# Optimization experiments

Hardware: AMD Instinct MI355X
Metric: run time of the kernel (lower is better)

Reference implementation:

```python
import jax, jax.numpy as jnp
import numpy as np

EMBED_DIM = 512
NUM_HEADS = 8
HEAD_DIM = EMBED_DIM // NUM_HEADS
N_NODES = 65536
EPS = 1e-5


def setup_inputs() -> dict:
    key = jax.random.key(0)
    ks = jax.random.split(key, 16)
    std = 0.02
    E, F = EMBED_DIM, 4 * EMBED_DIM
    return {
        "x": jax.random.normal(ks[0], (N_NODES, E), jnp.float32),
        "Wq": jax.random.normal(ks[1], (E, E), jnp.float32) * std,
        "bq": jnp.zeros((E,), jnp.float32),
        "Wk": jax.random.normal(ks[2], (E, E), jnp.float32) * std,
        "bk": jnp.zeros((E,), jnp.float32),
        "Wv": jax.random.normal(ks[3], (E, E), jnp.float32) * std,
        "bv": jnp.zeros((E,), jnp.float32),
        "Wo": jax.random.normal(ks[4], (E, E), jnp.float32) * std,
        "bo": jnp.zeros((E,), jnp.float32),
        "W1": jax.random.normal(ks[5], (F, E), jnp.float32) * std,
        "b1": jnp.zeros((F,), jnp.float32),
        "W2": jax.random.normal(ks[6], (E, F), jnp.float32) * std,
        "b2": jnp.zeros((E,), jnp.float32),
        "g1": jnp.ones((E,), jnp.float32),
        "beta1": jnp.zeros((E,), jnp.float32),
        "g2": jnp.ones((E,), jnp.float32),
        "beta2": jnp.zeros((E,), jnp.float32),
    }


def _layernorm(x, g, b):
    mu = jnp.mean(x, axis=-1, keepdims=True)
    var = jnp.mean(jnp.square(x - mu), axis=-1, keepdims=True)
    return (x - mu) * jax.lax.rsqrt(var + EPS) * g + b


def reference(x, Wq, bq, Wk, bk, Wv, bv, Wo, bo, W1, b1, W2, b2, g1, beta1, g2, beta2):
    N = x.shape[0]
    H, D = NUM_HEADS, HEAD_DIM
    residual = x
    h = _layernorm(x, g1, beta1)
    q = (h @ Wq.T + bq).reshape(N, H, D)
    k = (h @ Wk.T + bk).reshape(N, H, D)
    v = (h @ Wv.T + bv).reshape(N, H, D)
    # per-node attention across heads: scores (N, H, H)
    scores = jnp.einsum('nhd,ngd->nhg', q, k) / np.float32(np.sqrt(D))
    attn = jax.nn.softmax(scores, axis=-1)
    out = jnp.einsum('nhg,ngd->nhd', attn, v).reshape(N, H * D)
    out = out @ Wo.T + bo
    x = residual + out  # dropout is identity in eval
    residual = x
    h = _layernorm(x, g2, beta2)
    ff = jax.nn.relu(h @ W1.T + b1) @ W2.T + b2
    return residual + ff
```

## Files before the change

kernel.cpp:

```cpp
#include <hip/hip_runtime.h>
#include <hip/hip_bf16.h>
#include <stdint.h>

typedef __hip_bfloat16 bf16;
typedef short bf16x8 __attribute__((ext_vector_type(8)));
typedef float f32x4 __attribute__((ext_vector_type(4)));

typedef __attribute__((address_space(1))) const unsigned int as1_uint;
typedef __attribute__((address_space(3))) unsigned int as3_uint;

__device__ __forceinline__ void async_copy16(const void* g, void* l) {
    __builtin_amdgcn_global_load_lds((as1_uint*)g, (as3_uint*)l, 16, 0, 0);
}

__device__ __forceinline__ float b2f(unsigned short u) {
    union { unsigned int i; float f; } c; c.i = ((unsigned int)u) << 16; return c.f;
}
__device__ __forceinline__ unsigned short f2b(float f) {
    union { float f; unsigned int i; } c; c.f = f;
    unsigned int i = c.i;
    i += 0x7fffu + ((i >> 16) & 1u);
    return (unsigned short)(i >> 16);
}

__global__ __launch_bounds__(256)
void cvt_kernel(const float* __restrict__ in, bf16* __restrict__ out)
{
    const int i = (blockIdx.x * 256 + threadIdx.x) * 8;
    const float4 a = *(const float4*)(in + i);
    const float4 b = *(const float4*)(in + i + 4);
    union { uint4 v; unsigned short s[8]; } u;
    u.s[0] = f2b(a.x); u.s[1] = f2b(a.y); u.s[2] = f2b(a.z); u.s[3] = f2b(a.w);
    u.s[4] = f2b(b.x); u.s[5] = f2b(b.y); u.s[6] = f2b(b.z); u.s[7] = f2b(b.w);
    *(uint4*)((unsigned short*)out + i) = u.v;
}

__global__ __launch_bounds__(256)
void ln_kernel(const float* __restrict__ x, const float* __restrict__ g,
               const float* __restrict__ beta, bf16* __restrict__ out)
{
    const int w = threadIdx.x >> 6, l = threadIdx.x & 63;
    const int n = blockIdx.x * 4 + w;

    const float* xr = x + (size_t)n * 512 + l * 8;
    const float4 a = *(const float4*)xr;
    const float4 b = *(const float4*)(xr + 4);
    float f[8] = {a.x, a.y, a.z, a.w, b.x, b.y, b.z, b.w};

    float s = 0.f, q = 0.f;
#pragma unroll
    for (int i = 0; i < 8; ++i) { s += f[i]; q += f[i] * f[i]; }
#pragma unroll
    for (int o = 32; o > 0; o >>= 1) { s += __shfl_xor(s, o); q += __shfl_xor(q, o); }
    const float mean = s * (1.f / 512.f);
    const float var  = q * (1.f / 512.f) - mean * mean;
    const float rstd = rsqrtf(var + 1e-5f);

    const float4 g0 = *(const float4*)(g + l * 8);
    const float4 g1 = *(const float4*)(g + l * 8 + 4);
    const float4 b0 = *(const float4*)(beta + l * 8);
    const float4 b1 = *(const float4*)(beta + l * 8 + 4);
    const float gg[8] = {g0.x,g0.y,g0.z,g0.w,g1.x,g1.y,g1.z,g1.w};
    const float bb[8] = {b0.x,b0.y,b0.z,b0.w,b1.x,b1.y,b1.z,b1.w};

    union { uint4 v; unsigned short s[8]; } o;
#pragma unroll
    for (int i = 0; i < 8; ++i)
        o.s[i] = f2b((f[i] - mean) * rstd * gg[i] + bb[i]);
    *(uint4*)((unsigned short*)out + (size_t)n * 512 + l * 8) = o.v;
}

__global__ __launch_bounds__(256)
void attn_kernel(const bf16* __restrict__ qkv, bf16* __restrict__ out)
{
    __shared__ unsigned short sm[4][1536];
    const int w = threadIdx.x >> 6, l = threadIdx.x & 63;
    const int n = blockIdx.x * 4 + w;

    const uint4* src = (const uint4*)((const unsigned short*)qkv + (size_t)n * 1536);
    uint4* dst = (uint4*)sm[w];
#pragma unroll
    for (int i = 0; i < 3; ++i) dst[i * 64 + l] = src[i * 64 + l];
    __syncthreads();

    const int h = l >> 3, gi = l & 7;
    const unsigned short* qrow = sm[w] + h * 64;
    const unsigned short* krow = sm[w] + 512 + gi * 64;
    float s = 0.f;
#pragma unroll
    for (int jj = 0; jj < 8; ++jj) {
        union { uint4 v; unsigned short s8[8]; } qa, ka;
        qa.v = *(const uint4*)(qrow + jj * 8);
        ka.v = *(const uint4*)(krow + jj * 8);
#pragma unroll
        for (int j = 0; j < 8; ++j) s += b2f(qa.s8[j]) * b2f(ka.s8[j]);
    }
    s *= 0.125f;

    float m = s;
#pragma unroll
    for (int o = 1; o < 8; o <<= 1) m = fmaxf(m, __shfl_xor(m, o));
    float e = __expf(s - m);
    float d = e;
#pragma unroll
    for (int o = 1; o < 8; o <<= 1) d += __shfl_xor(d, o);
    const float p = e / d;

    float acc[8];
#pragma unroll
    for (int j = 0; j < 8; ++j) acc[j] = 0.f;
    const int j8 = (l & 7) * 8;
#pragma unroll
    for (int gg = 0; gg < 8; ++gg) {
        const float pg = __shfl(p, (l & 56) | gg);
        union { uint4 v; unsigned short s8[8]; } va;
        va.v = *(const uint4*)(sm[w] + 1024 + gg * 64 + j8);
#pragma unroll
        for (int j = 0; j < 8; ++j) acc[j] += pg * b2f(va.s8[j]);
    }
    union { uint4 v; unsigned short s8[8]; } o;
#pragma unroll
    for (int j = 0; j < 8; ++j) o.s8[j] = f2b(acc[j]);
    *(uint4*)((unsigned short*)out + (size_t)n * 512 + h * 64 + j8) = o.v;
}

#define EPI_PLAIN 0
#define EPI_RES   1
#define EPI_RELU  2

template<int MODE>
__global__ __launch_bounds__(512, 2)
void gemm_bt(const bf16* __restrict__ A,
             const bf16* __restrict__ B0, const bf16* __restrict__ B1,
             const bf16* __restrict__ B2,
             const float* __restrict__ bias0, const float* __restrict__ bias1,
             const float* __restrict__ bias2,
             const float* __restrict__ res,
             void* __restrict__ C,
             int K, int Nper, int ldc)
{
    __shared__ bf16 As[4][8192];
    __shared__ bf16 Bs[4][8192];

    const int tid = threadIdx.x;
    const int w = tid >> 6, l = tid & 63;

    const int nbx = gridDim.x;
    const int nwg = nbx * (int)gridDim.y;
    int lid = blockIdx.y * nbx + blockIdx.x;
    {
        const int q = nwg >> 3, r = nwg & 7;
        const int xcd = lid & 7, idx = lid >> 3;
        lid = (xcd < r ? xcd * (q + 1) : r * (q + 1) + (xcd - r) * q) + idx;
    }
    const int bx = lid % nbx, by = lid / nbx;

    const int rowBase = by * 256;
    const int colBase = bx * 256;
    const int sel = colBase / Nper;
    const bf16*  B    = (sel == 0) ? B0 : (sel == 1) ? B1 : B2;
    const float* bias = (sel == 0) ? bias0 : (sel == 1) ? bias1 : bias2;
    const int colInB = colBase - sel * Nper;

    const bf16* Ag = A + (size_t)rowBase * K;
    const bf16* Bg = B + (size_t)colInB * K;

    const int wr = w >> 2, wc = w & 3;
    const int ml = l & 15;
    const int kc = l >> 4;
    const int ac = ((kc ^ ((ml >> 1) & 3)) << 3);

    auto stage = [&](int t, int slot) {
        const int lr = l >> 2, lc = l & 3;
#pragma unroll
        for (int j = 0; j < 2; ++j) {
            const int cid = w * 2 + j;
            const int r = (cid << 4) + lr;
            const int c = lc ^ ((lr >> 1) & 3);
            const size_t go = (size_t)r * K + (t << 5) + (c << 3);
            async_copy16(Ag + go, &As[slot][cid << 9]);
            async_copy16(Bg + go, &Bs[slot][cid << 9]);
        }
    };

    f32x4 acc[8][4];
#pragma unroll
    for (int i = 0; i < 8; ++i)
#pragma unroll
        for (int j = 0; j < 4; ++j) acc[i][j] = (f32x4)(0.f);

    const int NT = K >> 5;

    stage(0, 0); stage(1, 1); stage(2, 2);
    asm volatile("s_waitcnt vmcnt(8)" ::: "memory");
    __builtin_amdgcn_s_barrier();

    for (int t = 0; t < NT; ++t) {
        if (t + 3 < NT) stage(t + 3, (t + 3) & 3);

        const bf16* Ac = &As[t & 3][0];
        const bf16* Bc = &Bs[t & 3][0];
        bf16x8 bfr[4];
#pragma unroll
        for (int ni = 0; ni < 4; ++ni)
            bfr[ni] = *(const bf16x8*)(Bc + (((wc << 6) + (ni << 4) + ml) << 5) + ac);

        __builtin_amdgcn_s_setprio(1);
#pragma unroll
        for (int mi = 0; mi < 8; ++mi) {
            const bf16x8 a = *(const bf16x8*)(Ac + (((wr << 7) + (mi << 4) + ml) << 5) + ac);
#pragma unroll
            for (int ni = 0; ni < 4; ++ni)
                acc[mi][ni] = __builtin_amdgcn_mfma_f32_16x16x32_bf16(
                    a, bfr[ni], acc[mi][ni], 0, 0, 0);
        }
        __builtin_amdgcn_s_setprio(0);

        if (t < NT - 3)       asm volatile("s_waitcnt vmcnt(8)" ::: "memory");
        else if (t == NT - 3) asm volatile("s_waitcnt vmcnt(4)" ::: "memory");
        else if (t == NT - 2) asm volatile("s_waitcnt vmcnt(0)" ::: "memory");
        if (t < NT - 1) __builtin_amdgcn_s_barrier();
    }

    float bv[4];
#pragma unroll
    for (int ni = 0; ni < 4; ++ni)
        bv[ni] = bias[colInB + (wc << 6) + (ni << 4) + ml];

#pragma unroll
    for (int mi = 0; mi < 8; ++mi) {
#pragma unroll
        for (int r4 = 0; r4 < 4; ++r4) {
            const int row = rowBase + (wr << 7) + (mi << 4) + (kc << 2) + r4;
            const size_t rowoff = (size_t)row * ldc;
#pragma unroll
            for (int ni = 0; ni < 4; ++ni) {
                const int gcol = colBase + (wc << 6) + (ni << 4) + ml;
                float v = acc[mi][ni][r4] + bv[ni];
                if (MODE == EPI_RELU) v = fmaxf(v, 0.f);
                if (MODE == EPI_RES) {
                    v += res[rowoff + gcol];
                    ((float*)C)[rowoff + gcol] = v;
                } else {
                    ((unsigned short*)C)[rowoff + gcol] = f2b(v);
                }
            }
        }
    }
}

extern "C" void kernel_launch(void* const* d_in, const int* in_sizes, int n_in,
                              void* d_out, int out_size, void* d_ws, size_t ws_size,
                              hipStream_t stream)
{
    const float* x   = (const float*)d_in[0];
    const float* Wq  = (const float*)d_in[1];
    const float* bq  = (const float*)d_in[2];
    const float* Wk  = (const float*)d_in[3];
    const float* bk  = (const float*)d_in[4];
    const float* Wv  = (const float*)d_in[5];
    const float* bv  = (const float*)d_in[6];
    const float* Wo  = (const float*)d_in[7];
    const float* bo  = (const float*)d_in[8];
    const float* W1  = (const float*)d_in[9];
    const float* b1  = (const float*)d_in[10];
    const float* W2  = (const float*)d_in[11];
    const float* b2  = (const float*)d_in[12];
    const float* g1  = (const float*)d_in[13];
    const float* be1 = (const float*)d_in[14];
    const float* g2  = (const float*)d_in[15];
    const float* be2 = (const float*)d_in[16];

    const int N = 65536;

    bf16* Wqb = (bf16*)d_ws;
    bf16* Wkb = Wqb + 262144;
    bf16* Wvb = Wkb + 262144;
    bf16* Wob = Wvb + 262144;
    bf16* W1b = Wob + 262144;
    bf16* W2b = W1b + 1048576;
    const size_t wts_bytes = 6ull * 1024 * 1024;
    bf16* t64 = (bf16*)((char*)d_ws + wts_bytes);
    const size_t t64_bytes = (size_t)N * 512 * 2;
    bf16* cb  = (bf16*)((char*)d_ws + wts_bytes + t64_bytes);
    const size_t used = wts_bytes + t64_bytes;
    const size_t avail = ws_size > used ? ws_size - used : 0;
    int Nc = 32768;
    while (Nc > 256 && (size_t)Nc * 4096 > avail) Nc >>= 1;

    float* x2 = (float*)d_out;
    dim3 blk(256);
    dim3 blk5(512);

    cvt_kernel<<<262144 / 2048, blk, 0, stream>>>(Wq, Wqb);
    cvt_kernel<<<262144 / 2048, blk, 0, stream>>>(Wk, Wkb);
    cvt_kernel<<<262144 / 2048, blk, 0, stream>>>(Wv, Wvb);
    cvt_kernel<<<262144 / 2048, blk, 0, stream>>>(Wo, Wob);
    cvt_kernel<<<1048576 / 2048, blk, 0, stream>>>(W1, W1b);
    cvt_kernel<<<1048576 / 2048, blk, 0, stream>>>(W2, W2b);

    ln_kernel<<<N / 4, blk, 0, stream>>>(x, g1, be1, t64);

    for (int r0 = 0; r0 < N; r0 += Nc) {
        gemm_bt<EPI_PLAIN><<<dim3(6, Nc / 256), blk5, 0, stream>>>(
            t64 + (size_t)r0 * 512, Wqb, Wkb, Wvb, bq, bk, bv, nullptr,
            cb, 512, 512, 1536);
        attn_kernel<<<Nc / 4, blk, 0, stream>>>(cb, t64 + (size_t)r0 * 512);
    }

    gemm_bt<EPI_RES><<<dim3(2, N / 256), blk5, 0, stream>>>(
        t64, Wob, Wob, Wob, bo, bo, bo, x, x2, 512, 512, 512);

    ln_kernel<<<N / 4, blk, 0, stream>>>(x2, g2, be2, t64);

    for (int r0 = 0; r0 < N; r0 += Nc) {
        gemm_bt<EPI_RELU><<<dim3(8, Nc / 256), blk5, 0, stream>>>(
            t64 + (size_t)r0 * 512, W1b, W1b, W1b, b1, b1, b1, nullptr,
            cb, 512, 2048, 2048);
        gemm_bt<EPI_RES><<<dim3(2, Nc / 256), blk5, 0, stream>>>(
            cb, W2b, W2b, W2b, b2, b2, b2, x2 + (size_t)r0 * 512,
            x2 + (size_t)r0 * 512, 2048, 512, 512);
    }
}
```

Before: 1.052 ms.

## Split GEMM main loop into two interleaved load/prefetch/MFMA phases

Restructures the bf16 GEMM inner loop into two halves. Each half loads its A fragments from LDS, issues half of the next-tile async global→LDS prefetch, then runs a barrier-synchronised MFMA cluster, in the style of ping-pong scheduling. The aim is to interleave memory issue with matrix compute and let waves alternate between memory and MFMA phases. It adds extra workgroup barriers per K-step, which could cost more than the overlap gains.

```diff
diff --git a/kernel.cpp b/kernel.cpp
--- a/kernel.cpp
+++ b/kernel.cpp
@@ -170,17 +170,14 @@
     const int kc = l >> 4;
     const int ac = ((kc ^ ((ml >> 1) & 3)) << 3);
 
-    auto stage = [&](int t, int slot) {
+    auto stage_half = [&](int t, int slot, int j) {
         const int lr = l >> 2, lc = l & 3;
-#pragma unroll
-        for (int j = 0; j < 2; ++j) {
-            const int cid = w * 2 + j;
-            const int r = (cid << 4) + lr;
-            const int c = lc ^ ((lr >> 1) & 3);
-            const size_t go = (size_t)r * K + (t << 5) + (c << 3);
-            async_copy16(Ag + go, &As[slot][cid << 9]);
-            async_copy16(Bg + go, &Bs[slot][cid << 9]);
-        }
+        const int cid = w * 2 + j;
+        const int r = (cid << 4) + lr;
+        const int c = lc ^ ((lr >> 1) & 3);
+        const size_t go = (size_t)r * K + (t << 5) + (c << 3);
+        async_copy16(Ag + go, &As[slot][cid << 9]);
+        async_copy16(Bg + go, &Bs[slot][cid << 9]);
     };
 
     f32x4 acc[8][4];
@@ -191,29 +188,54 @@
 
     const int NT = K >> 5;
 
-    stage(0, 0); stage(1, 1); stage(2, 2);
+    stage_half(0, 0, 0); stage_half(0, 0, 1);
+    stage_half(1, 1, 0); stage_half(1, 1, 1);
+    stage_half(2, 2, 0); stage_half(2, 2, 1);
     asm volatile("s_waitcnt vmcnt(8)" ::: "memory");
     __builtin_amdgcn_s_barrier();
 
     for (int t = 0; t < NT; ++t) {
-        if (t + 3 < NT) stage(t + 3, (t + 3) & 3);
-
-        const bf16* Ac = &As[t & 3][0];
-        const bf16* Bc = &Bs[t & 3][0];
-        bf16x8 bfr[4];
+        const int slot = t & 3;
+        const bf16* Ac = &As[slot][0];
+        const bf16* Bc = &Bs[slot][0];
+        const bool pf = (t + 3 < NT);
+
+        bf16x8 bfr[4], af[4];
 #pragma unroll
         for (int ni = 0; ni < 4; ++ni)
             bfr[ni] = *(const bf16x8*)(Bc + (((wc << 6) + (ni << 4) + ml) << 5) + ac);
-
+#pragma unroll
+        for (int mi = 0; mi < 4; ++mi)
+            af[mi] = *(const bf16x8*)(Ac + (((wr << 7) + (mi << 4) + ml) << 5) + ac);
+        if (pf) stage_half(t + 3, (t + 3) & 3, 0);
+
+        __builtin_amdgcn_s_barrier();
+        asm volatile("s_waitcnt lgkmcnt(0)" ::: "memory");
         __builtin_amdgcn_s_setprio(1);
 #pragma unroll
-        for (int mi = 0; mi < 8; ++mi) {
-            const bf16x8 a = *(const bf16x8*)(Ac + (((wr << 7) + (mi << 4) + ml) << 5) + ac);
+        for (int mi = 0; mi < 4; ++mi)
 #pragma unroll
             for (int ni = 0; ni < 4; ++ni)
                 acc[mi][ni] = __builtin_amdgcn_mfma_f32_16x16x32_bf16(
-                    a, bfr[ni], acc[mi][ni], 0, 0, 0);
-        }
+                    af[mi], bfr[ni], acc[mi][ni], 0, 0, 0);
+        __builtin_amdgcn_s_setprio(0);
+        __builtin_amdgcn_s_barrier();
+
+        bf16x8 ag[4];
+#pragma unroll
+        for (int mi = 0; mi < 4; ++mi)
+            ag[mi] = *(const bf16x8*)(Ac + (((wr << 7) + ((mi + 4) << 4) + ml) << 5) + ac);
+        if (pf) stage_half(t + 3, (t + 3) & 3, 1);
+
+        __builtin_amdgcn_s_barrier();
+        asm volatile("s_waitcnt lgkmcnt(0)" ::: "memory");
+        __builtin_amdgcn_s_setprio(1);
+#pragma unroll
+        for (int mi = 0; mi < 4; ++mi)
+#pragma unroll
+            for (int ni = 0; ni < 4; ++ni)
+                acc[mi + 4][ni] = __builtin_amdgcn_mfma_f32_16x16x32_bf16(
+                    ag[mi], bfr[ni], acc[mi + 4][ni], 0, 0, 0);
         __builtin_amdgcn_s_setprio(0);
 
         if (t < NT - 3)       asm volatile("s_waitcnt vmcnt(8)" ::: "memory");
```

Result: faster. 985.4 us (-6.3%).

## Shrink GEMM tiles to 128x128 with 256 threads and 3-stage pipeline

Applied to the files above, without the earlier changes.

Reworks the bf16 GEMM from 256x256 tiles on 512 threads with a 4-slot, 3-ahead async LDS pipeline to 128x128 tiles on 256 threads with a 3-slot, 2-ahead pipeline. A fragments are now preloaded per k-step. Launch grids double in each dimension. The aim is a smaller LDS footprint (48KB vs 128KB) and more workgroups per CU to raise occupancy and hide latency. The cost is lower arithmetic intensity per tile, so each output needs more global/L2 traffic, plus a shallower prefetch.

```diff
diff --git a/kernel.cpp b/kernel.cpp
--- a/kernel.cpp
+++ b/kernel.cpp
@@ -129,7 +129,7 @@
 #define EPI_RELU  2
 
 template<int MODE>
-__global__ __launch_bounds__(512, 2)
+__global__ __launch_bounds__(256, 3)
 void gemm_bt(const bf16* __restrict__ A,
              const bf16* __restrict__ B0, const bf16* __restrict__ B1,
              const bf16* __restrict__ B2,
@@ -139,8 +139,8 @@
              void* __restrict__ C,
              int K, int Nper, int ldc)
 {
-    __shared__ bf16 As[4][8192];
-    __shared__ bf16 Bs[4][8192];
+    __shared__ bf16 As[3][4096];
+    __shared__ bf16 Bs[3][4096];
 
     const int tid = threadIdx.x;
     const int w = tid >> 6, l = tid & 63;
@@ -155,8 +155,8 @@
     }
     const int bx = lid % nbx, by = lid / nbx;
 
-    const int rowBase = by * 256;
-    const int colBase = bx * 256;
+    const int rowBase = by * 128;
+    const int colBase = bx * 128;
     const int sel = colBase / Nper;
     const bf16*  B    = (sel == 0) ? B0 : (sel == 1) ? B1 : B2;
     const float* bias = (sel == 0) ? bias0 : (sel == 1) ? bias1 : bias2;
@@ -165,61 +165,63 @@
     const bf16* Ag = A + (size_t)rowBase * K;
     const bf16* Bg = B + (size_t)colInB * K;
 
-    const int wr = w >> 2, wc = w & 3;
+    const int wr = w >> 1, wc = w & 1;
     const int ml = l & 15;
-    const int kc = l >> 4;
-    const int ac = ((kc ^ ((ml >> 1) & 3)) << 3);
+    const int ac = (((l >> 4) ^ ((ml >> 1) & 3)) << 3);
 
     auto stage = [&](int t, int slot) {
         const int lr = l >> 2, lc = l & 3;
-#pragma unroll
-        for (int j = 0; j < 2; ++j) {
-            const int cid = w * 2 + j;
-            const int r = (cid << 4) + lr;
-            const int c = lc ^ ((lr >> 1) & 3);
-            const size_t go = (size_t)r * K + (t << 5) + (c << 3);
-            async_copy16(Ag + go, &As[slot][cid << 9]);
-            async_copy16(Bg + go, &Bs[slot][cid << 9]);
+        const int c = lc ^ ((lr >> 1) & 3);
+#pragma unroll
+        for (int i = 0; i < 2; ++i) {
+            const int base = w * 32 + i * 16;
+            const size_t go = (size_t)(base + lr) * K + (t << 5) + (c << 3);
+            async_copy16(Ag + go, &As[slot][base << 5]);
+            async_copy16(Bg + go, &Bs[slot][base << 5]);
         }
     };
 
-    f32x4 acc[8][4];
-#pragma unroll
-    for (int i = 0; i < 8; ++i)
+    f32x4 acc[4][4];
+#pragma unroll
+    for (int i = 0; i < 4; ++i)
 #pragma unroll
         for (int j = 0; j < 4; ++j) acc[i][j] = (f32x4)(0.f);
 
     const int NT = K >> 5;
 
-    stage(0, 0); stage(1, 1); stage(2, 2);
-    asm volatile("s_waitcnt vmcnt(8)" ::: "memory");
+    stage(0, 0); stage(1, 1);
+    asm volatile("s_waitcnt vmcnt(4)" ::: "memory");
     __builtin_amdgcn_s_barrier();
 
+    int slot = 0, pslot = 2;
     for (int t = 0; t < NT; ++t) {
-        if (t + 3 < NT) stage(t + 3, (t + 3) & 3);
-
-        const bf16* Ac = &As[t & 3][0];
-        const bf16* Bc = &Bs[t & 3][0];
-        bf16x8 bfr[4];
+        if (t + 2 < NT) stage(t + 2, pslot);
+
+        const bf16* Ac = &As[slot][0];
+        const bf16* Bc = &Bs[slot][0];
+        bf16x8 af[4], bfr[4];
+#pragma unroll
+        for (int mi = 0; mi < 4; ++mi)
+            af[mi] = *(const bf16x8*)(Ac + (((wr << 6) + (mi << 4) + ml) << 5) + ac);
 #pragma unroll
         for (int ni = 0; ni < 4; ++ni)
             bfr[ni] = *(const bf16x8*)(Bc + (((wc << 6) + (ni << 4) + ml) << 5) + ac);
 
         __builtin_amdgcn_s_setprio(1);
 #pragma unroll
-        for (int mi = 0; mi < 8; ++mi) {
-            const bf16x8 a = *(const bf16x8*)(Ac + (((wr << 7) + (mi << 4) + ml) << 5) + ac);
+        for (int mi = 0; mi < 4; ++mi)
 #pragma unroll
             for (int ni = 0; ni < 4; ++ni)
                 acc[mi][ni] = __builtin_amdgcn_mfma_f32_16x16x32_bf16(
-                    a, bfr[ni], acc[mi][ni], 0, 0, 0);
-        }
+                    af[mi], bfr[ni], acc[mi][ni], 0, 0, 0);
         __builtin_amdgcn_s_setprio(0);
 
-        if (t < NT - 3)       asm volatile("s_waitcnt vmcnt(8)" ::: "memory");
-        else if (t == NT - 3) asm volatile("s_waitcnt vmcnt(4)" ::: "memory");
+        if (t + 2 < NT)       asm volatile("s_waitcnt vmcnt(4)" ::: "memory");
         else if (t == NT - 2) asm volatile("s_waitcnt vmcnt(0)" ::: "memory");
         if (t < NT - 1) __builtin_amdgcn_s_barrier();
+
+        slot  = (slot  == 2) ? 0 : slot + 1;
+        pslot = (pslot == 2) ? 0 : pslot + 1;
     }
 
     float bv[4];
@@ -228,10 +230,10 @@
         bv[ni] = bias[colInB + (wc << 6) + (ni << 4) + ml];
 
 #pragma unroll
-    for (int mi = 0; mi < 8; ++mi) {
+    for (int mi = 0; mi < 4; ++mi) {
 #pragma unroll
         for (int r4 = 0; r4 < 4; ++r4) {
-            const int row = rowBase + (wr << 7) + (mi << 4) + (kc << 2) + r4;
+            const int row = rowBase + (wr << 6) + (mi << 4) + ((l >> 4) << 2) + r4;
             const size_t rowoff = (size_t)row * ldc;
 #pragma unroll
             for (int ni = 0; ni < 4; ++ni) {
@@ -290,7 +292,6 @@
 
     float* x2 = (float*)d_out;
     dim3 blk(256);
-    dim3 blk5(512);
 
     cvt_kernel<<<262144 / 2048, blk, 0, stream>>>(Wq, Wqb);
     cvt_kernel<<<262144 / 2048, blk, 0, stream>>>(Wk, Wkb);
@@ -302,22 +303,22 @@
     ln_kernel<<<N / 4, blk, 0, stream>>>(x, g1, be1, t64);
 
     for (int r0 = 0; r0 < N; r0 += Nc) {
-        gemm_bt<EPI_PLAIN><<<dim3(6, Nc / 256), blk5, 0, stream>>>(
+        gemm_bt<EPI_PLAIN><<<dim3(12, Nc / 128), blk, 0, stream>>>(
             t64 + (size_t)r0 * 512, Wqb, Wkb, Wvb, bq, bk, bv, nullptr,
             cb, 512, 512, 1536);
         attn_kernel<<<Nc / 4, blk, 0, stream>>>(cb, t64 + (size_t)r0 * 512);
     }
 
-    gemm_bt<EPI_RES><<<dim3(2, N / 256), blk5, 0, stream>>>(
+    gemm_bt<EPI_RES><<<dim3(4, N / 128), blk, 0, stream>>>(
         t64, Wob, Wob, Wob, bo, bo, bo, x, x2, 512, 512, 512);
 
     ln_kernel<<<N / 4, blk, 0, stream>>>(x2, g2, be2, t64);
 
     for (int r0 = 0; r0 < N; r0 += Nc) {
-        gemm_bt<EPI_RELU><<<dim3(8, Nc / 256), blk5, 0, stream>>>(
+        gemm_bt<EPI_RELU><<<dim3(16, Nc / 128), blk, 0, stream>>>(
             t64 + (size_t)r0 * 512, W1b, W1b, W1b, b1, b1, b1, nullptr,
             cb, 512, 2048, 2048);
-        gemm_bt<EPI_RES><<<dim3(2, Nc / 256), blk5, 0, stream>>>(
+        gemm_bt<EPI_RES><<<dim3(4, Nc / 128), blk, 0, stream>>>(
             cb, W2b, W2b, W2b, b2, b2, b2, x2 + (size_t)r0 * 512,
             x2 + (size_t)r0 * 512, 2048, 512, 512);
     }
```

Measured after the change: 1.018 ms. -3.2%, faster.

## Restructure GEMM mainloop into 8-phase ping-pong schedule with 64-wide K tiles

Applied to the files above, without the earlier changes.

The bf16 GEMM mainloop moves from a 4-slot, 32-wide K pipeline to a double-buffered 64-wide K tile split into A/B halves. Each K step is broken into quadrant phases, each with its own LDS fragment loads, async global-to-LDS prefetch, barriers and an MFMA burst, in the style of a ping-pong schedule. The aim is to hide global-load and LDS latency behind matrix work and to halve the loop trip count. It adds more barriers, fragile vmcnt accounting and higher register pressure from the fragment arrays.

```diff
diff --git a/kernel.cpp b/kernel.cpp
--- a/kernel.cpp
+++ b/kernel.cpp
@@ -139,8 +139,8 @@
              void* __restrict__ C,
              int K, int Nper, int ldc)
 {
-    __shared__ bf16 As[4][8192];
-    __shared__ bf16 Bs[4][8192];
+    __shared__ bf16 As[2][2][8192];
+    __shared__ bf16 Bs[2][2][8192];
 
     const int tid = threadIdx.x;
     const int w = tid >> 6, l = tid & 63;
@@ -168,20 +168,34 @@
     const int wr = w >> 2, wc = w & 3;
     const int ml = l & 15;
     const int kc = l >> 4;
-    const int ac = ((kc ^ ((ml >> 1) & 3)) << 3);
-
-    auto stage = [&](int t, int slot) {
-        const int lr = l >> 2, lc = l & 3;
-#pragma unroll
-        for (int j = 0; j < 2; ++j) {
-            const int cid = w * 2 + j;
-            const int r = (cid << 4) + lr;
-            const int c = lc ^ ((lr >> 1) & 3);
-            const size_t go = (size_t)r * K + (t << 5) + (c << 3);
-            async_copy16(Ag + go, &As[slot][cid << 9]);
-            async_copy16(Bg + go, &Bs[slot][cid << 9]);
+    const int rdoff = ((kc ^ ((ml >> 1) & 3)) << 3);
+
+    const int s_row = l >> 2;
+    const int s_koff = (((l & 3) ^ ((l >> 3) & 3)) << 3);
+
+    auto stA = [&](int t, int half) {
+#pragma unroll
+        for (int c = 0; c < 2; ++c) {
+            const int q = (w << 1) | c;
+            const int p = q >> 3, rr = q & 7;
+            const bf16* src = Ag + (size_t)(half * 128 + rr * 16 + s_row) * K
+                            + (t << 6) + p * 32 + s_koff;
+            async_copy16(src, &As[t & 1][half][q << 9]);
         }
     };
+    auto stB = [&](int t, int half) {
+#pragma unroll
+        for (int c = 0; c < 2; ++c) {
+            const int q = (w << 1) | c;
+            const int p = q >> 3, rr = q & 7;
+            const bf16* src = Bg + (size_t)(half * 128 + rr * 16 + s_row) * K
+                            + (t << 6) + p * 32 + s_koff;
+            async_copy16(src, &Bs[t & 1][half][q << 9]);
+        }
+    };
+
+    const int bRow = ((wc & 1) << 6) + ml;
+    const int bHalf = wc >> 1;
 
     f32x4 acc[8][4];
 #pragma unroll
@@ -189,37 +203,105 @@
 #pragma unroll
         for (int j = 0; j < 4; ++j) acc[i][j] = (f32x4)(0.f);
 
-    const int NT = K >> 5;
-
-    stage(0, 0); stage(1, 1); stage(2, 2);
-    asm volatile("s_waitcnt vmcnt(8)" ::: "memory");
+    bf16x8 af[4][2], bf[4][2];
+
+#define LDA(SLOT, MI, KS) \
+    (*(const bf16x8*)(&As[SLOT][wr][(KS) * 4096 + ((MI) * 16 + ml) * 32 + rdoff]))
+#define LDB(SLOT, NI, KS) \
+    (*(const bf16x8*)(&Bs[SLOT][bHalf][(KS) * 4096 + (bRow + (NI) * 16) * 32 + rdoff]))
+
+#define MMQ(MG, NG) \
+    do { \
+        _Pragma("unroll") \
+        for (int mi = 0; mi < 4; ++mi) \
+        _Pragma("unroll") \
+        for (int nj = 0; nj < 2; ++nj) \
+        _Pragma("unroll") \
+        for (int ks = 0; ks < 2; ++ks) \
+            acc[(MG)*4+mi][(NG)*2+nj] = __builtin_amdgcn_mfma_f32_16x16x32_bf16( \
+                af[mi][ks], bf[(NG)*2+nj][ks], acc[(MG)*4+mi][(NG)*2+nj], 0, 0, 0); \
+    } while (0)
+
+#define SYNC_IN()  do { __builtin_amdgcn_s_barrier(); \
+                        __builtin_amdgcn_sched_barrier(0); \
+                        asm volatile("s_waitcnt lgkmcnt(0)" ::: "memory"); \
+                        __builtin_amdgcn_sched_barrier(0); } while (0)
+#define SYNC_OUT() do { __builtin_amdgcn_s_barrier(); \
+                        __builtin_amdgcn_sched_barrier(0); } while (0)
+
+    const int NT = K >> 6;
+    const int NI = NT >> 1;
+
+    stA(0, 0); stA(0, 1); stB(0, 0); stB(0, 1);
+    stA(1, 0); stB(1, 0);
+    asm volatile("s_waitcnt vmcnt(4)" ::: "memory");
     __builtin_amdgcn_s_barrier();
-
-    for (int t = 0; t < NT; ++t) {
-        if (t + 3 < NT) stage(t + 3, (t + 3) & 3);
-
-        const bf16* Ac = &As[t & 3][0];
-        const bf16* Bc = &Bs[t & 3][0];
-        bf16x8 bfr[4];
-#pragma unroll
-        for (int ni = 0; ni < 4; ++ni)
-            bfr[ni] = *(const bf16x8*)(Bc + (((wc << 6) + (ni << 4) + ml) << 5) + ac);
-
-        __builtin_amdgcn_s_setprio(1);
-#pragma unroll
-        for (int mi = 0; mi < 8; ++mi) {
-            const bf16x8 a = *(const bf16x8*)(Ac + (((wr << 7) + (mi << 4) + ml) << 5) + ac);
-#pragma unroll
-            for (int ni = 0; ni < 4; ++ni)
-                acc[mi][ni] = __builtin_amdgcn_mfma_f32_16x16x32_bf16(
-                    a, bfr[ni], acc[mi][ni], 0, 0, 0);
-        }
-        __builtin_amdgcn_s_setprio(0);
-
-        if (t < NT - 3)       asm volatile("s_waitcnt vmcnt(8)" ::: "memory");
-        else if (t == NT - 3) asm volatile("s_waitcnt vmcnt(4)" ::: "memory");
-        else if (t == NT - 2) asm volatile("s_waitcnt vmcnt(0)" ::: "memory");
-        if (t < NT - 1) __builtin_amdgcn_s_barrier();
+    __builtin_amdgcn_sched_barrier(0);
+
+    for (int i = 0; i < NI; ++i) {
+        const int t1 = 2 * i + 1;
+        const bool pf = (t1 + 1 < NT);
+
+#pragma unroll
+        for (int mi = 0; mi < 4; ++mi) { af[mi][0] = LDA(0, mi, 0); af[mi][1] = LDA(0, mi, 1); }
+#pragma unroll
+        for (int nj = 0; nj < 2; ++nj) { bf[nj][0] = LDB(0, nj, 0); bf[nj][1] = LDB(0, nj, 1); }
+        stA(t1, 1);
+        SYNC_IN();
+        __builtin_amdgcn_s_setprio(1); MMQ(0, 0); __builtin_amdgcn_s_setprio(0);
+        SYNC_OUT();
+
+#pragma unroll
+        for (int nj = 2; nj < 4; ++nj) { bf[nj][0] = LDB(0, nj, 0); bf[nj][1] = LDB(0, nj, 1); }
+        stB(t1, 1);
+        SYNC_IN();
+        __builtin_amdgcn_s_setprio(1); MMQ(0, 1); __builtin_amdgcn_s_setprio(0);
+        SYNC_OUT();
+
+#pragma unroll
+        for (int mi = 0; mi < 4; ++mi) { af[mi][0] = LDA(0, mi + 4, 0); af[mi][1] = LDA(0, mi + 4, 1); }
+        if (pf) stB(t1 + 1, 0);
+        SYNC_IN();
+        __builtin_amdgcn_s_setprio(1); MMQ(1, 0); __builtin_amdgcn_s_setprio(0);
+        SYNC_OUT();
+
+        if (pf) stB(t1 + 1, 1);
+        __builtin_amdgcn_s_barrier();
+        __builtin_amdgcn_sched_barrier(0);
+        __builtin_amdgcn_s_setprio(1); MMQ(1, 1); __builtin_amdgcn_s_setprio(0);
+        if (pf) asm volatile("s_waitcnt vmcnt(4)" ::: "memory");
+        else    asm volatile("s_waitcnt vmcnt(0)" ::: "memory");
+        SYNC_OUT();
+
+#pragma unroll
+        for (int mi = 0; mi < 4; ++mi) { af[mi][0] = LDA(1, mi, 0); af[mi][1] = LDA(1, mi, 1); }
+#pragma unroll
+        for (int nj = 0; nj < 2; ++nj) { bf[nj][0] = LDB(1, nj, 0); bf[nj][1] = LDB(1, nj, 1); }
+        if (pf) stA(t1 + 1, 0);
+        SYNC_IN();
+        __builtin_amdgcn_s_setprio(1); MMQ(0, 0); __builtin_amdgcn_s_setprio(0);
+        SYNC_OUT();
+
+#pragma unroll
+        for (int nj = 2; nj < 4; ++nj) { bf[nj][0] = LDB(1, nj, 0); bf[nj][1] = LDB(1, nj, 1); }
+        if (pf) stA(t1 + 1, 1);
+        SYNC_IN();
+        __builtin_amdgcn_s_setprio(1); MMQ(0, 1); __builtin_amdgcn_s_setprio(0);
+        SYNC_OUT();
+
+#pragma unroll
+        for (int mi = 0; mi < 4; ++mi) { af[mi][0] = LDA(1, mi + 4, 0); af[mi][1] = LDA(1, mi + 4, 1); }
+        if (pf) stB(t1 + 2, 0);
+        SYNC_IN();
+        __builtin_amdgcn_s_setprio(1); MMQ(1, 0); __builtin_amdgcn_s_setprio(0);
+        SYNC_OUT();
+
+        if (pf) stA(t1 + 2, 0);
+        __builtin_amdgcn_s_barrier();
+        __builtin_amdgcn_sched_barrier(0);
+        __builtin_amdgcn_s_setprio(1); MMQ(1, 1); __builtin_amdgcn_s_setprio(0);
+        if (pf) asm volatile("s_waitcnt vmcnt(4)" ::: "memory");
+        if (i < NI - 1) SYNC_OUT();
     }
 
     float bv[4];
@@ -247,6 +329,11 @@
             }
         }
     }
+#undef LDA
+#undef LDB
+#undef MMQ
+#undef SYNC_IN
+#undef SYNC_OUT
 }
 
 extern "C" void kernel_launch(void* const* d_in, const int* in_sizes, int n_in,
```

Result: faster. 925.5 us (-12.0%).
